# Kernel optimization log

Hardware: AMD Instinct MI355X
Metric: run time of the kernel (lower is better)

Reference implementation:

```python
import jax, jax.numpy as jnp
import numpy as np


def setup_inputs() -> dict:
    key = jax.random.key(0)
    k1, k2, k3, k4 = jax.random.split(key, 4)
    B, Q, K, H, D = 2, 2048, 2048, 16, 128
    qs = jax.random.normal(k1, (B, Q, H, D), dtype=jnp.float32)
    ks = jax.random.normal(k2, (B, K, H, D), dtype=jnp.float32)
    vs = jax.random.normal(k3, (B, K, H, D), dtype=jnp.float32)
    valid_lens = jax.random.randint(k4, (B,), 1, K + 1, dtype=jnp.int32)
    return {"qs": qs, "ks": ks, "vs": vs, "valid_lens": valid_lens}


def reference(qs, ks, vs, valid_lens):
    B, Q, H, D = qs.shape
    K = ks.shape[1]
    # rearrange 'B L H D -> (B H) L D'
    q = qs.transpose(0, 2, 1, 3).reshape(B * H, Q, D)
    k = ks.transpose(0, 2, 1, 3).reshape(B * H, K, D)
    v = vs.transpose(0, 2, 1, 3).reshape(B * H, K, D)
    # DotScorer: scaled dot product -> (B*H, Q, K)
    scores = jnp.einsum('bqd,bkd->bqk', q, k) / jnp.sqrt(jnp.float32(D))
    # mask_attn: key positions >= valid_len get large negative score
    vl = jnp.repeat(valid_lens, H)                         # (B*H,)
    mask = jnp.arange(K)[None, None, :] < vl[:, None, None]
    scores = jnp.where(mask, scores, jnp.float32(-1e6))
    attn = jax.nn.softmax(scores, axis=-1)
    # dropout is identity (p_dropout=0 / not training)
    ctx = attn @ v                                         # (B*H, Q, D)
    ctx = ctx.reshape(B, H, Q, D).transpose(0, 2, 1, 3)    # (B, Q, H, D)
    return ctx, attn.reshape(B, H, Q, K)
```

## Files before the change

kernel.cpp:

```cpp
#include <hip/hip_runtime.h>
#include <hip/hip_bf16.h>
#include <stdint.h>

#define B_ 2
#define Qn 2048
#define Kn 2048
#define Hn 16
#define Dn 128
#define QT 128
#define KT 64
#define KT1 128
#define HD (Hn*Dn)

typedef __bf16 bf16x8 __attribute__((ext_vector_type(8)));
typedef __bf16 bf16x4 __attribute__((ext_vector_type(4)));
typedef float f32x4 __attribute__((ext_vector_type(4)));
typedef float f32x16 __attribute__((ext_vector_type(16)));
typedef unsigned short u16x8 __attribute__((ext_vector_type(8)));

union BF8 { __bf16 e[8]; bf16x8 v; };
union U16x8 { unsigned short u[8]; u16x8 v; };

#define SCALE 0.088388347648318447f
#define SCL2  (0.088388347648318447f * 1.4426950408889634f)

#if __has_builtin(__builtin_amdgcn_exp2f)
#define EXP2(x) __builtin_amdgcn_exp2f(x)
#else
#define EXP2(x) exp2f(x)
#endif

__device__ __forceinline__ bf16x4 cvt4(f32x4 a) {
  bf16x4 r;
  r[0] = (__bf16)a[0]; r[1] = (__bf16)a[1];
  r[2] = (__bf16)a[2]; r[3] = (__bf16)a[3];
  return r;
}

__global__ __launch_bounds__(256) void conv_k(const float* __restrict__ ks,
                                              unsigned short* __restrict__ kws) {
  const int blk = blockIdx.x;
  const int bh = blk >> 4, t = blk & 15;
  const int b = bh >> 4, h = bh & 15;
  const int tid = threadIdx.x;
  const float* src = ks + ((size_t)(b * Kn + t * 128) * Hn + h) * Dn;
  unsigned short* dst = kws + (size_t)blk * 16384;
  #pragma unroll
  for (int i = 0; i < 8; ++i) {
    int idx = i * 256 + tid;
    int row = idx >> 4, sp = idx & 15;
    int slot = (sp - row) & 15;
    const float* s2 = src + (size_t)row * HD + slot * 8;
    f32x4 a0 = *(const f32x4*)s2;
    f32x4 a1 = *(const f32x4*)(s2 + 4);
    U16x8 o;
    *(bf16x4*)&o.u[0] = cvt4(a0);
    *(bf16x4*)&o.u[4] = cvt4(a1);
    *(u16x8*)(dst + (size_t)idx * 8) = o.v;
  }
}

__global__ __launch_bounds__(256) void conv_v(const float* __restrict__ vs,
                                              unsigned short* __restrict__ vws) {
  __shared__ unsigned short l[64 * 132];
  const int blk = blockIdx.x;
  const int bh = blk >> 5, t = blk & 31;
  const int b = bh >> 4, h = bh & 15;
  const int tid = threadIdx.x;
  const float* src = vs + ((size_t)(b * Kn + t * 64) * Hn + h) * Dn;
  #pragma unroll
  for (int i = 0; i < 8; ++i) {
    int idx = i * 256 + tid;
    int k = idx >> 5, dc = idx & 31;
    f32x4 a = *(const f32x4*)(src + (size_t)k * HD + dc * 4);
    *(bf16x4*)&l[k * 132 + dc * 4] = cvt4(a);
  }
  __syncthreads();
  unsigned short* dst = vws + (size_t)blk * 8192;
  #pragma unroll
  for (int i = 0; i < 4; ++i) {
    int idx = i * 256 + tid;
    int d = idx >> 3, ds = idx & 7;
    int c = (ds - d) & 7;
    int kb = ((c >> 2) * 32) + (((c >> 1) & 1) * 16) + ((c & 1) * 4);
    U16x8 o;
    #pragma unroll
    for (int j = 0; j < 4; ++j) {
      o.u[j]     = l[(kb + j) * 132 + d];
      o.u[4 + j] = l[(kb + 8 + j) * 132 + d];
    }
    *(u16x8*)(dst + (size_t)idx * 8) = o.v;
  }
}

__device__ __forceinline__ void dma16(const void* g, void* l) {
  __builtin_amdgcn_global_load_lds((const __attribute__((address_space(1))) void*)g,
                                   (__attribute__((address_space(3))) void*)l, 16, 0, 0);
}
__device__ __forceinline__ void dma_tile(const char* gsrc, char* lds, int tid, int n4k) {
  const int off  = tid * 16;
  const int woff = (tid & 192) * 16;
  #pragma unroll
  for (int i = 0; i < n4k; ++i)
    dma16(gsrc + i * 4096 + off, lds + i * 4096 + woff);
}

#define WAIT0BAR do { \
  asm volatile("s_waitcnt vmcnt(0)" ::: "memory"); \
  __builtin_amdgcn_s_barrier(); \
  __builtin_amdgcn_sched_barrier(0); } while (0)

#define WAIT8BAR do { \
  asm volatile("s_waitcnt vmcnt(8)" ::: "memory"); \
  __builtin_amdgcn_s_barrier(); \
  __builtin_amdgcn_sched_barrier(0); } while (0)

__global__ __launch_bounds__(256, 2) void attn_fwd(
    const float* __restrict__ qs, const int* __restrict__ vlen,
    const char* __restrict__ kimg, const char* __restrict__ vimg,
    float* __restrict__ ctx_out, float* __restrict__ attn_out)
{
  __shared__ __align__(16) char smraw[65536];

  const int tid = threadIdx.x, wave = tid >> 6, lane = tid & 63;
  const int l31 = lane & 31, hi = lane >> 5;

  const int L   = blockIdx.x;
  const int xcd = L & 7;
  const int i5  = L >> 3;
  const int bh  = ((i5 & 3) << 3) + xcd;
  const int qt  = i5 >> 2;
  const int b   = bh >> 4, h = bh & 15;
  const int vl  = vlen[b];
  const int qbw = qt * QT + wave * 32;

  int vaddrK[8], vaddrV[4];
  #pragma unroll
  for (int s = 0; s < 8; ++s)
    vaddrK[s] = l31 * 256 + (((2 * s + hi + l31) & 15) << 4);
  #pragma unroll
  for (int j = 0; j < 4; ++j)
    vaddrV[j] = l31 * 128 + ((((hi + 2 * j) + l31) & 7) << 4);

  BF8 qf[8];
  {
    const float* qrow = qs + (((size_t)(b * Qn + qbw + l31)) * Hn + h) * Dn;
    #pragma unroll
    for (int s = 0; s < 8; ++s) {
      int d0 = s * 16 + hi * 8;
      f32x4 a0 = *(const f32x4*)(qrow + d0);
      f32x4 a1 = *(const f32x4*)(qrow + d0 + 4);
      #pragma unroll
      for (int j = 0; j < 4; ++j) {
        qf[s].e[j]     = (__bf16)(a0[j] * SCL2);
        qf[s].e[4 + j] = (__bf16)(a1[j] * SCL2);
      }
    }
  }

  const char* kimg_bh = kimg + ((size_t)(bh * 16) << 15);
  const char* vimg_bh = vimg + ((size_t)(bh * 32) << 14);

  const int nkt  = (vl + KT - 1) / KT;
  const int col0 = nkt * KT;

  f32x4 rsv = {0.f, 0.f, 0.f, 0.f};
  {
    const int nkt1 = (vl + KT1 - 1) / KT1;
    const bool hasb1 = (vl & (KT1 - 1)) != 0;
    dma_tile(kimg_bh, smraw, tid, 8);
    WAIT0BAR;
    for (int t = 0; t < nkt1; ++t) {
      const int cur = t & 1;
      if (t + 1 < nkt1) dma_tile(kimg_bh + ((size_t)(t + 1) << 15), smraw + ((cur ^ 1) << 15), tid, 8);
      #pragma unroll 1
      for (int r = t; r < 32; r += nkt1) {
        float* zp = attn_out + ((size_t)bh * Qn + qbw + r) * Kn;
        for (int c4 = col0 + lane * 4; c4 < Kn; c4 += 256)
          *(f32x4*)(zp + c4) = (f32x4){0.f, 0.f, 0.f, 0.f};
      }
      const bool mb = hasb1 && (t == nkt1 - 1);
      const char* kb_l = smraw + (cur << 15);
      #pragma unroll
      for (int m = 0; m < 4; ++m) {
        f32x16 acc;
        #pragma unroll
        for (int i = 0; i < 16; ++i) acc[i] = 0.f;
        #pragma unroll
        for (int s = 0; s < 8; ++s) {
          BF8 kf; kf.v = *(const bf16x8*)(kb_l + m * 8192 + vaddrK[s]);
          acc = __builtin_amdgcn_mfma_f32_32x32x16_bf16(kf.v, qf[s].v, acc, 0, 0, 0);
        }
        if (!mb) {
          #pragma unroll
          for (int reg = 0; reg < 16; ++reg) rsv[reg & 3] += EXP2(acc[reg]);
        } else {
          const int kb0 = t * KT1 + m * 32 + hi * 4;
          #pragma unroll
          for (int reg = 0; reg < 16; ++reg) {
            int key = kb0 + (reg & 3) + 8 * (reg >> 2);
            rsv[reg & 3] += (key < vl) ? EXP2(acc[reg]) : 0.f;
          }
        }
      }
      WAIT0BAR;
    }
  }
  float rs = (rsv[0] + rsv[1]) + (rsv[2] + rsv[3]);
  rs += __shfl_xor(rs, 32);
  const float inv = 1.0f / rs;

  f32x16 ctxa[4];
  #pragma unroll
  for (int ch = 0; ch < 4; ++ch)
    #pragma unroll
    for (int i = 0; i < 16; ++i) ctxa[ch][i] = 0.f;

  const bool hasb2 = (vl & (KT - 1)) != 0;
  dma_tile(kimg_bh, smraw, tid, 4);
  dma_tile(vimg_bh, smraw + 32768, tid, 4);
  WAIT0BAR;
  float* rowp = attn_out + ((size_t)bh * Qn + qbw + l31) * Kn;
  for (int t = 0; t < nkt; ++t) {
    const int cur = t & 1;
    if (t + 1 < nkt) {
      const int tn = t + 1;
      dma_tile(kimg_bh + ((size_t)(tn >> 1) << 15) + ((size_t)(tn & 1) << 14),
               smraw + ((cur ^ 1) << 14), tid, 4);
      dma_tile(vimg_bh + ((size_t)tn << 14), smraw + 32768 + ((cur ^ 1) << 14), tid, 4);
    }
    const bool mb = hasb2 && (t == nkt - 1);
    const char* kb_l = smraw + (cur << 14);
    const char* vb_l = smraw + 32768 + (cur << 14);
    #pragma unroll
    for (int m = 0; m < 2; ++m) {
      f32x16 acc;
      #pragma unroll
      for (int i = 0; i < 16; ++i) acc[i] = 0.f;
      #pragma unroll
      for (int s = 0; s < 8; ++s) {
        BF8 kf; kf.v = *(const bf16x8*)(kb_l + m * 8192 + vaddrK[s]);
        acc = __builtin_amdgcn_mfma_f32_32x32x16_bf16(kf.v, qf[s].v, acc, 0, 0, 0);
      }
      const int kb0 = t * KT + m * 32;
      BF8 pf0, pf1;
      #pragma unroll
      for (int r4 = 0; r4 < 4; ++r4) {
        f32x4 p;
        if (!mb) {
          #pragma unroll
          for (int rr = 0; rr < 4; ++rr) p[rr] = EXP2(acc[r4 * 4 + rr]) * inv;
        } else {
          #pragma unroll
          for (int rr = 0; rr < 4; ++rr) {
            int key = kb0 + r4 * 8 + hi * 4 + rr;
            p[rr] = (key < vl) ? EXP2(acc[r4 * 4 + rr]) * inv : 0.f;
          }
        }
        #pragma unroll
        for (int rr = 0; rr < 4; ++rr) {
          if (r4 < 2) pf0.e[r4 * 4 + rr] = (__bf16)p[rr];
          else        pf1.e[(r4 - 2) * 4 + rr] = (__bf16)p[rr];
        }
        *(f32x4*)(rowp + kb0 + r4 * 8 + hi * 4) = p;
      }
      #pragma unroll
      for (int ch = 0; ch < 4; ++ch) {
        BF8 v0; v0.v = *(const bf16x8*)(vb_l + ch * 4096 + vaddrV[2 * m]);
        ctxa[ch] = __builtin_amdgcn_mfma_f32_32x32x16_bf16(v0.v, pf0.v, ctxa[ch], 0, 0, 0);
        BF8 v1; v1.v = *(const bf16x8*)(vb_l + ch * 4096 + vaddrV[2 * m + 1]);
        ctxa[ch] = __builtin_amdgcn_mfma_f32_32x32x16_bf16(v1.v, pf1.v, ctxa[ch], 0, 0, 0);
      }
    }
    WAIT8BAR;
  }

  float* cp = ctx_out + (((size_t)(b * Qn + qbw + l31)) * Hn + h) * Dn;
  #pragma unroll
  for (int ch = 0; ch < 4; ++ch)
    #pragma unroll
    for (int r4 = 0; r4 < 4; ++r4) {
      f32x4 o;
      #pragma unroll
      for (int rr = 0; rr < 4; ++rr) o[rr] = ctxa[ch][r4 * 4 + rr];
      *(f32x4*)(cp + ch * 32 + r4 * 8 + hi * 4) = o;
    }
}

#define KROW 132
#define VROW 72
struct SMp2f { unsigned short K[2][KT][KROW]; unsigned short V[2][Dn][VROW]; };
union SMuf { SMp2f p2; unsigned short K1[2][KT1][KROW]; };

__device__ __forceinline__ void bar_lgkm() {
  asm volatile("s_waitcnt lgkmcnt(0)" ::: "memory");
  __builtin_amdgcn_s_barrier();
  __builtin_amdgcn_sched_barrier(0);
}
__device__ __forceinline__ void fb_stage_k64(const float* kb, unsigned short (*dst)[KROW], int tid) {
  #pragma unroll
  for (int ii = 0; ii < 8; ++ii) {
    int chunk = ii * 256 + tid;
    int row = chunk >> 5, cv = chunk & 31;
    f32x4 a = *(const f32x4*)(kb + (size_t)row * HD + cv * 4);
    *(bf16x4*)&dst[row][cv * 4] = cvt4(a);
  }
}
__device__ __forceinline__ void fb_stage_k128(const float* kb, unsigned short (*dst)[KROW], int tid) {
  #pragma unroll
  for (int ii = 0; ii < 16; ++ii) {
    int chunk = ii * 256 + tid;
    int row = chunk >> 5, cv = chunk & 31;
    f32x4 a = *(const f32x4*)(kb + (size_t)row * HD + cv * 4);
    *(bf16x4*)&dst[row][cv * 4] = cvt4(a);
  }
}
__device__ __forceinline__ void fb_stage_v64(const float* vb, unsigned short (*dst)[VROW], int tid) {
  int d = tid & 127, t0 = tid >> 7;
  const float* colp = vb + d;
  #pragma unroll
  for (int rr = 0; rr < 4; ++rr) {
    int idx = rr * 2 + t0;
    int base = (idx >> 2) * 32 + ((idx >> 1) & 1) * 16 + (idx & 1) * 4;
    BF8 t;
    #pragma unroll
    for (int j = 0; j < 4; ++j) {
      t.e[j]     = (__bf16)colp[(size_t)(base + j) * HD];
      t.e[4 + j] = (__bf16)colp[(size_t)(base + 8 + j) * HD];
    }
    *(bf16x8*)&dst[d][idx * 8] = t.v;
  }
}
__global__ __launch_bounds__(256, 2) void attn_fwd_fb(
    const float* __restrict__ qs, const float* __restrict__ ks,
    const float* __restrict__ vs, const int* __restrict__ vlen,
    float* __restrict__ ctx_out, float* __restrict__ attn_out)
{
  __shared__ __align__(16) SMuf sm;
  const int tid = threadIdx.x, wave = tid >> 6, lane = tid & 63;
  const int l31 = lane & 31, hi = lane >> 5;
  const int L = blockIdx.x, xcd = L & 7, i5 = L >> 3;
  const int bh = ((i5 & 3) << 3) + xcd, qt = i5 >> 2;
  const int b = bh >> 4, h = bh & 15;
  const int vl = vlen[b];
  const int qbw = qt * QT + wave * 32;
  BF8 qf[8];
  {
    const float* qrow = qs + (((size_t)(b * Qn + qbw + l31)) * Hn + h) * Dn;
    #pragma unroll
    for (int s = 0; s < 8; ++s) {
      int d0 = s * 16 + hi * 8;
      f32x4 a0 = *(const f32x4*)(qrow + d0);
      f32x4 a1 = *(const f32x4*)(qrow + d0 + 4);
      #pragma unroll
      for (int j = 0; j < 4; ++j) {
        qf[s].e[j] = (__bf16)(a0[j] * SCL2);
        qf[s].e[4 + j] = (__bf16)(a1[j] * SCL2);
      }
    }
  }
  const float* kbase = ks + ((size_t)b * Kn * Hn + h) * Dn;
  const float* vbase = vs + ((size_t)b * Kn * Hn + h) * Dn;
  f32x4 rsv = {0.f, 0.f, 0.f, 0.f};
  {
    const int nkt1 = (vl + KT1 - 1) / KT1;
    const bool hasb1 = (vl & (KT1 - 1)) != 0;
    fb_stage_k128(kbase, sm.K1[0], tid);
    bar_lgkm();
    for (int t = 0; t < nkt1; ++t) {
      const int cur = t & 1;
      if (t + 1 < nkt1) fb_stage_k128(kbase + (size_t)(t + 1) * KT1 * HD, sm.K1[cur ^ 1], tid);
      const bool mb = hasb1 && (t == nkt1 - 1);
      #pragma unroll
      for (int m = 0; m < 4; ++m) {
        f32x16 acc;
        #pragma unroll
        for (int i = 0; i < 16; ++i) acc[i] = 0.f;
        #pragma unroll
        for (int s = 0; s < 8; ++s) {
          BF8 kf; kf.v = *(const bf16x8*)&sm.K1[cur][m * 32 + l31][s * 16 + hi * 8];
          acc = __builtin_amdgcn_mfma_f32_32x32x16_bf16(kf.v, qf[s].v, acc, 0, 0, 0);
        }
        if (!mb) {
          #pragma unroll
          for (int reg = 0; reg < 16; ++reg) rsv[reg & 3] += EXP2(acc[reg]);
        } else {
          const int kb0 = t * KT1 + m * 32 + hi * 4;
          #pragma unroll
          for (int reg = 0; reg < 16; ++reg) {
            int key = kb0 + (reg & 3) + 8 * (reg >> 2);
            rsv[reg & 3] += (key < vl) ? EXP2(acc[reg]) : 0.f;
          }
        }
      }
      bar_lgkm();
    }
  }
  float rs = (rsv[0] + rsv[1]) + (rsv[2] + rsv[3]);
  rs += __shfl_xor(rs, 32);
  const float inv = 1.0f / rs;
  f32x16 ctxa[4];
  #pragma unroll
  for (int ch = 0; ch < 4; ++ch)
    #pragma unroll
    for (int i = 0; i < 16; ++i) ctxa[ch][i] = 0.f;
  const int nkt = (vl + KT - 1) / KT;
  const bool hasb2 = (vl & (KT - 1)) != 0;
  fb_stage_k64(kbase, sm.p2.K[0], tid);
  fb_stage_v64(vbase, sm.p2.V[0], tid);
  bar_lgkm();
  float* rowp = attn_out + ((size_t)bh * Qn + qbw + l31) * Kn;
  for (int t = 0; t < nkt; ++t) {
    const int cur = t & 1;
    if (t + 1 < nkt) {
      fb_stage_k64(kbase + (size_t)(t + 1) * KT * HD, sm.p2.K[cur ^ 1], tid);
      fb_stage_v64(vbase + (size_t)(t + 1) * KT * HD, sm.p2.V[cur ^ 1], tid);
    }
    const bool mb = hasb2 && (t == nkt - 1);
    #pragma unroll
    for (int m = 0; m < 2; ++m) {
      f32x16 acc;
      #pragma unroll
      for (int i = 0; i < 16; ++i) acc[i] = 0.f;
      #pragma unroll
      for (int s = 0; s < 8; ++s) {
        BF8 kf; kf.v = *(const bf16x8*)&sm.p2.K[cur][m * 32 + l31][s * 16 + hi * 8];
        acc = __builtin_amdgcn_mfma_f32_32x32x16_bf16(kf.v, qf[s].v, acc, 0, 0, 0);
      }
      const int kb0 = t * KT + m * 32;
      BF8 pf0, pf1;
      #pragma unroll
      for (int r4 = 0; r4 < 4; ++r4) {
        f32x4 p;
        if (!mb) {
          #pragma unroll
          for (int rr = 0; rr < 4; ++rr) p[rr] = EXP2(acc[r4 * 4 + rr]) * inv;
        } else {
          #pragma unroll
          for (int rr = 0; rr < 4; ++rr) {
            int key = kb0 + r4 * 8 + hi * 4 + rr;
            p[rr] = (key < vl) ? EXP2(acc[r4 * 4 + rr]) * inv : 0.f;
          }
        }
        #pragma unroll
        for (int rr = 0; rr < 4; ++rr) {
          if (r4 < 2) pf0.e[r4 * 4 + rr] = (__bf16)p[rr];
          else        pf1.e[(r4 - 2) * 4 + rr] = (__bf16)p[rr];
        }
        *(f32x4*)(rowp + kb0 + r4 * 8 + hi * 4) = p;
      }
      #pragma unroll
      for (int ch = 0; ch < 4; ++ch) {
        BF8 v0; v0.v = *(const bf16x8*)&sm.p2.V[cur][ch * 32 + l31][(m * 4 + hi) * 8];
        ctxa[ch] = __builtin_amdgcn_mfma_f32_32x32x16_bf16(v0.v, pf0.v, ctxa[ch], 0, 0, 0);
        BF8 v1; v1.v = *(const bf16x8*)&sm.p2.V[cur][ch * 32 + l31][(m * 4 + 2 + hi) * 8];
        ctxa[ch] = __builtin_amdgcn_mfma_f32_32x32x16_bf16(v1.v, pf1.v, ctxa[ch], 0, 0, 0);
      }
    }
    bar_lgkm();
  }
  const int col0 = nkt * KT;
  #pragma unroll 1
  for (int r = 0; r < 32; ++r) {
    float* zp = attn_out + ((size_t)bh * Qn + qbw + r) * Kn;
    for (int c4 = col0 + lane * 4; c4 < Kn; c4 += 256)
      *(f32x4*)(zp + c4) = (f32x4){0.f, 0.f, 0.f, 0.f};
  }
  float* cp = ctx_out + (((size_t)(b * Qn + qbw + l31)) * Hn + h) * Dn;
  #pragma unroll
  for (int ch = 0; ch < 4; ++ch)
    #pragma unroll
    for (int r4 = 0; r4 < 4; ++r4) {
      f32x4 o;
      #pragma unroll
      for (int rr = 0; rr < 4; ++rr) o[rr] = ctxa[ch][r4 * 4 + rr];
      *(f32x4*)(cp + ch * 32 + r4 * 8 + hi * 4) = o;
    }
}

extern "C" void kernel_launch(void* const* d_in, const int* in_sizes, int n_in,
                              void* d_out, int out_size, void* d_ws, size_t ws_size,
                              hipStream_t stream) {
  const float* qs   = (const float*)d_in[0];
  const float* ks   = (const float*)d_in[1];
  const float* vs   = (const float*)d_in[2];
  const int*   vlen = (const int*)d_in[3];
  float* ctx  = (float*)d_out;
  float* attn = ctx + (size_t)B_ * Qn * Hn * Dn;

  if (ws_size >= ((size_t)32 << 20)) {
    unsigned short* kws = (unsigned short*)d_ws;
    unsigned short* vws = kws + ((size_t)8 << 20);
    conv_k<<<dim3(512), 256, 0, stream>>>(ks, kws);
    conv_v<<<dim3(1024), 256, 0, stream>>>(vs, vws);
    attn_fwd<<<dim3((Qn / QT) * B_ * Hn), 256, 0, stream>>>(
        qs, vlen, (const char*)kws, (const char*)vws, ctx, attn);
  } else {
    attn_fwd_fb<<<dim3((Qn / QT) * B_ * Hn), 256, 0, stream>>>(qs, ks, vs, vlen, ctx, attn);
  }
}
```

Measured before the change: 199.6 us.

## Move PV accumulation into first softmax pass and skip conversion of masked key tiles

The P·V MFMA accumulation now runs in the first pass on unnormalized exponentials, alongside the row-sum computation, and the context is scaled by 1/rowsum at the end. The second pass only recomputes QK scores with 128-key tiles and writes the normalized attention matrix, so it no longer loads V. The K and V bf16 conversion kernels also skip tiles beyond the valid length. This rebalances the two passes and cuts conversion traffic. In exchange, pass one now carries extra V loads and MFMAs, and unnormalized bf16 probabilities could change precision slightly.

```diff
diff --git a/kernel.cpp b/kernel.cpp
--- a/kernel.cpp
+++ b/kernel.cpp
@@ -8,8 +8,6 @@
 #define Hn 16
 #define Dn 128
 #define QT 128
-#define KT 64
-#define KT1 128
 #define HD (Hn*Dn)
 
 typedef __bf16 bf16x8 __attribute__((ext_vector_type(8)));
@@ -38,10 +36,13 @@
 }
 
 __global__ __launch_bounds__(256) void conv_k(const float* __restrict__ ks,
+                                              const int* __restrict__ vlen,
                                               unsigned short* __restrict__ kws) {
   const int blk = blockIdx.x;
   const int bh = blk >> 4, t = blk & 15;
   const int b = bh >> 4, h = bh & 15;
+  const int nkt = (vlen[b] + 63) >> 6;
+  if (t * 2 >= nkt) return;
   const int tid = threadIdx.x;
   const float* src = ks + ((size_t)(b * Kn + t * 128) * Hn + h) * Dn;
   unsigned short* dst = kws + (size_t)blk * 16384;
@@ -61,11 +62,14 @@
 }
 
 __global__ __launch_bounds__(256) void conv_v(const float* __restrict__ vs,
+                                              const int* __restrict__ vlen,
                                               unsigned short* __restrict__ vws) {
   __shared__ unsigned short l[64 * 132];
   const int blk = blockIdx.x;
   const int bh = blk >> 5, t = blk & 31;
   const int b = bh >> 4, h = bh & 15;
+  const int nkt = (vlen[b] + 63) >> 6;
+  if (t >= nkt) return;
   const int tid = threadIdx.x;
   const float* src = vs + ((size_t)(b * Kn + t * 64) * Hn + h) * Dn;
   #pragma unroll
@@ -110,8 +114,8 @@
   __builtin_amdgcn_s_barrier(); \
   __builtin_amdgcn_sched_barrier(0); } while (0)
 
-#define WAIT8BAR do { \
-  asm volatile("s_waitcnt vmcnt(8)" ::: "memory"); \
+#define WAIT16BAR do { \
+  asm volatile("s_waitcnt vmcnt(16)" ::: "memory"); \
   __builtin_amdgcn_s_barrier(); \
   __builtin_amdgcn_sched_barrier(0); } while (0)
 
@@ -161,28 +165,41 @@
   const char* kimg_bh = kimg + ((size_t)(bh * 16) << 15);
   const char* vimg_bh = vimg + ((size_t)(bh * 32) << 14);
 
-  const int nkt  = (vl + KT - 1) / KT;
-  const int col0 = nkt * KT;
+  const int nkt  = (vl + 63) >> 6;
+  const int nkt2 = (vl + 127) >> 7;
+  const int col0 = nkt * 64;
 
   f32x4 rsv = {0.f, 0.f, 0.f, 0.f};
+  f32x16 ctxa[4];
+  #pragma unroll
+  for (int ch = 0; ch < 4; ++ch)
+    #pragma unroll
+    for (int i = 0; i < 16; ++i) ctxa[ch][i] = 0.f;
+
   {
-    const int nkt1 = (vl + KT1 - 1) / KT1;
-    const bool hasb1 = (vl & (KT1 - 1)) != 0;
-    dma_tile(kimg_bh, smraw, tid, 8);
+    const bool hasb = (vl & 63) != 0;
+    dma_tile(kimg_bh, smraw, tid, 4);
+    dma_tile(vimg_bh, smraw + 32768, tid, 4);
     WAIT0BAR;
-    for (int t = 0; t < nkt1; ++t) {
+    for (int t = 0; t < nkt; ++t) {
       const int cur = t & 1;
-      if (t + 1 < nkt1) dma_tile(kimg_bh + ((size_t)(t + 1) << 15), smraw + ((cur ^ 1) << 15), tid, 8);
+      if (t + 1 < nkt) {
+        const int tn = t + 1;
+        dma_tile(kimg_bh + ((size_t)(tn >> 1) << 15) + ((size_t)(tn & 1) << 14),
+                 smraw + ((cur ^ 1) << 14), tid, 4);
+        dma_tile(vimg_bh + ((size_t)tn << 14), smraw + 32768 + ((cur ^ 1) << 14), tid, 4);
+      }
       #pragma unroll 1
-      for (int r = t; r < 32; r += nkt1) {
+      for (int r = t; r < 32; r += nkt) {
         float* zp = attn_out + ((size_t)bh * Qn + qbw + r) * Kn;
         for (int c4 = col0 + lane * 4; c4 < Kn; c4 += 256)
           *(f32x4*)(zp + c4) = (f32x4){0.f, 0.f, 0.f, 0.f};
       }
-      const bool mb = hasb1 && (t == nkt1 - 1);
-      const char* kb_l = smraw + (cur << 15);
-      #pragma unroll
-      for (int m = 0; m < 4; ++m) {
+      const bool mb = hasb && (t == nkt - 1);
+      const char* kb_l = smraw + (cur << 14);
+      const char* vb_l = smraw + 32768 + (cur << 14);
+      #pragma unroll
+      for (int m = 0; m < 2; ++m) {
         f32x16 acc;
         #pragma unroll
         for (int i = 0; i < 16; ++i) acc[i] = 0.f;
@@ -191,16 +208,29 @@
           BF8 kf; kf.v = *(const bf16x8*)(kb_l + m * 8192 + vaddrK[s]);
           acc = __builtin_amdgcn_mfma_f32_32x32x16_bf16(kf.v, qf[s].v, acc, 0, 0, 0);
         }
-        if (!mb) {
+        const int kb0 = t * 64 + m * 32;
+        BF8 pf0, pf1;
+        #pragma unroll
+        for (int r4 = 0; r4 < 4; ++r4) {
           #pragma unroll
-          for (int reg = 0; reg < 16; ++reg) rsv[reg & 3] += EXP2(acc[reg]);
-        } else {
-          const int kb0 = t * KT1 + m * 32 + hi * 4;
-          #pragma unroll
-          for (int reg = 0; reg < 16; ++reg) {
-            int key = kb0 + (reg & 3) + 8 * (reg >> 2);
-            rsv[reg & 3] += (key < vl) ? EXP2(acc[reg]) : 0.f;
+          for (int rr = 0; rr < 4; ++rr) {
+            float e;
+            if (!mb) e = EXP2(acc[r4 * 4 + rr]);
+            else {
+              int key = kb0 + r4 * 8 + hi * 4 + rr;
+              e = (key < vl) ? EXP2(acc[r4 * 4 + rr]) : 0.f;
+            }
+            rsv[rr] += e;
+            if (r4 < 2) pf0.e[r4 * 4 + rr] = (__bf16)e;
+            else        pf1.e[(r4 - 2) * 4 + rr] = (__bf16)e;
           }
+        }
+        #pragma unroll
+        for (int ch = 0; ch < 4; ++ch) {
+          BF8 v0; v0.v = *(const bf16x8*)(vb_l + ch * 4096 + vaddrV[2 * m]);
+          ctxa[ch] = __builtin_amdgcn_mfma_f32_32x32x16_bf16(v0.v, pf0.v, ctxa[ch], 0, 0, 0);
+          BF8 v1; v1.v = *(const bf16x8*)(vb_l + ch * 4096 + vaddrV[2 * m + 1]);
+          ctxa[ch] = __builtin_amdgcn_mfma_f32_32x32x16_bf16(v1.v, pf1.v, ctxa[ch], 0, 0, 0);
         }
       }
       WAIT0BAR;
@@ -210,69 +240,46 @@
   rs += __shfl_xor(rs, 32);
   const float inv = 1.0f / rs;
 
-  f32x16 ctxa[4];
-  #pragma unroll
-  for (int ch = 0; ch < 4; ++ch)
-    #pragma unroll
-    for (int i = 0; i < 16; ++i) ctxa[ch][i] = 0.f;
-
-  const bool hasb2 = (vl & (KT - 1)) != 0;
-  dma_tile(kimg_bh, smraw, tid, 4);
-  dma_tile(vimg_bh, smraw + 32768, tid, 4);
-  WAIT0BAR;
-  float* rowp = attn_out + ((size_t)bh * Qn + qbw + l31) * Kn;
-  for (int t = 0; t < nkt; ++t) {
-    const int cur = t & 1;
-    if (t + 1 < nkt) {
-      const int tn = t + 1;
-      dma_tile(kimg_bh + ((size_t)(tn >> 1) << 15) + ((size_t)(tn & 1) << 14),
-               smraw + ((cur ^ 1) << 14), tid, 4);
-      dma_tile(vimg_bh + ((size_t)tn << 14), smraw + 32768 + ((cur ^ 1) << 14), tid, 4);
-    }
-    const bool mb = hasb2 && (t == nkt - 1);
-    const char* kb_l = smraw + (cur << 14);
-    const char* vb_l = smraw + 32768 + (cur << 14);
-    #pragma unroll
-    for (int m = 0; m < 2; ++m) {
-      f32x16 acc;
-      #pragma unroll
-      for (int i = 0; i < 16; ++i) acc[i] = 0.f;
-      #pragma unroll
-      for (int s = 0; s < 8; ++s) {
-        BF8 kf; kf.v = *(const bf16x8*)(kb_l + m * 8192 + vaddrK[s]);
-        acc = __builtin_amdgcn_mfma_f32_32x32x16_bf16(kf.v, qf[s].v, acc, 0, 0, 0);
-      }
-      const int kb0 = t * KT + m * 32;
-      BF8 pf0, pf1;
-      #pragma unroll
-      for (int r4 = 0; r4 < 4; ++r4) {
-        f32x4 p;
-        if (!mb) {
-          #pragma unroll
-          for (int rr = 0; rr < 4; ++rr) p[rr] = EXP2(acc[r4 * 4 + rr]) * inv;
-        } else {
-          #pragma unroll
-          for (int rr = 0; rr < 4; ++rr) {
-            int key = kb0 + r4 * 8 + hi * 4 + rr;
-            p[rr] = (key < vl) ? EXP2(acc[r4 * 4 + rr]) * inv : 0.f;
+  {
+    const bool hasb2 = (vl & 127) != 0;
+    dma_tile(kimg_bh, smraw, tid, 8);
+    WAIT0BAR;
+    float* rowp = attn_out + ((size_t)bh * Qn + qbw + l31) * Kn;
+    for (int t = 0; t < nkt2; ++t) {
+      const int cur = t & 1;
+      if (t + 1 < nkt2)
+        dma_tile(kimg_bh + ((size_t)(t + 1) << 15), smraw + ((cur ^ 1) << 15), tid, 8);
+      const bool mb = hasb2 && (t == nkt2 - 1);
+      const char* kb_l = smraw + (cur << 15);
+      #pragma unroll
+      for (int m = 0; m < 4; ++m) {
+        f32x16 acc;
+        #pragma unroll
+        for (int i = 0; i < 16; ++i) acc[i] = 0.f;
+        #pragma unroll
+        for (int s = 0; s < 8; ++s) {
+          BF8 kf; kf.v = *(const bf16x8*)(kb_l + m * 8192 + vaddrK[s]);
+          acc = __builtin_amdgcn_mfma_f32_32x32x16_bf16(kf.v, qf[s].v, acc, 0, 0, 0);
+        }
+        const int kb0 = t * 128 + m * 32;
+        #pragma unroll
+        for (int r4 = 0; r4 < 4; ++r4) {
+          f32x4 p;
+          if (!mb) {
+            #pragma unroll
+            for (int rr = 0; rr < 4; ++rr) p[rr] = EXP2(acc[r4 * 4 + rr]) * inv;
+          } else {
+            #pragma unroll
+            for (int rr = 0; rr < 4; ++rr) {
+              int key = kb0 + r4 * 8 + hi * 4 + rr;
+              p[rr] = (key < vl) ? EXP2(acc[r4 * 4 + rr]) * inv : 0.f;
+            }
           }
-        }
-        #pragma unroll
-        for (int rr = 0; rr < 4; ++rr) {
-          if (r4 < 2) pf0.e[r4 * 4 + rr] = (__bf16)p[rr];
-          else        pf1.e[(r4 - 2) * 4 + rr] = (__bf16)p[rr];
-        }
-        *(f32x4*)(rowp + kb0 + r4 * 8 + hi * 4) = p;
-      }
-      #pragma unroll
-      for (int ch = 0; ch < 4; ++ch) {
-        BF8 v0; v0.v = *(const bf16x8*)(vb_l + ch * 4096 + vaddrV[2 * m]);
-        ctxa[ch] = __builtin_amdgcn_mfma_f32_32x32x16_bf16(v0.v, pf0.v, ctxa[ch], 0, 0, 0);
-        BF8 v1; v1.v = *(const bf16x8*)(vb_l + ch * 4096 + vaddrV[2 * m + 1]);
-        ctxa[ch] = __builtin_amdgcn_mfma_f32_32x32x16_bf16(v1.v, pf1.v, ctxa[ch], 0, 0, 0);
-      }
-    }
-    WAIT8BAR;
+          *(f32x4*)(rowp + kb0 + r4 * 8 + hi * 4) = p;
+        }
+      }
+      WAIT16BAR;
+    }
   }
 
   float* cp = ctx_out + (((size_t)(b * Qn + qbw + l31)) * Hn + h) * Dn;
@@ -282,11 +289,13 @@
     for (int r4 = 0; r4 < 4; ++r4) {
       f32x4 o;
       #pragma unroll
-      for (int rr = 0; rr < 4; ++rr) o[rr] = ctxa[ch][r4 * 4 + rr];
+      for (int rr = 0; rr < 4; ++rr) o[rr] = ctxa[ch][r4 * 4 + rr] * inv;
       *(f32x4*)(cp + ch * 32 + r4 * 8 + hi * 4) = o;
     }
 }
 
+#define KT 64
+#define KT1 128
 #define KROW 132
 #define VROW 72
 struct SMp2f { unsigned short K[2][KT][KROW]; unsigned short V[2][Dn][VROW]; };
@@ -491,8 +500,8 @@
   if (ws_size >= ((size_t)32 << 20)) {
     unsigned short* kws = (unsigned short*)d_ws;
     unsigned short* vws = kws + ((size_t)8 << 20);
-    conv_k<<<dim3(512), 256, 0, stream>>>(ks, kws);
-    conv_v<<<dim3(1024), 256, 0, stream>>>(vs, vws);
+    conv_k<<<dim3(512), 256, 0, stream>>>(ks, vlen, kws);
+    conv_v<<<dim3(1024), 256, 0, stream>>>(vs, vlen, vws);
     attn_fwd<<<dim3((Qn / QT) * B_ * Hn), 256, 0, stream>>>(
         qs, vlen, (const char*)kws, (const char*)vws, ctx, attn);
   } else {
```

After: 188.5 us. -5.6%, faster.
